# Performance work log

Measured on AMD Instinct MI355X. Metric: run time of the kernel, lower is better.

The kernel has to match this reference:

```python
import jax, jax.numpy as jnp
import numpy as np

DN = ('NCHW', 'OIHW', 'NCHW')

def conv2d(x, w, b, stride, pad):
    y = jax.lax.conv_general_dilated(x, w, (stride, stride), ((pad, pad), (pad, pad)), dimension_numbers=DN)
    return y + b[None, :, None, None]

def conv_transpose2d(x, w, b, stride, pad):
    # w in PyTorch ConvTranspose2d layout: (in_ch, out_ch, kH, kW)
    k = w.shape[2]
    wf = jnp.transpose(w, (1, 0, 2, 3))[:, :, ::-1, ::-1]  # flipped, OIHW
    p = k - 1 - pad
    y = jax.lax.conv_general_dilated(x, wf, (1, 1), ((p, p), (p, p)), lhs_dilation=(stride, stride), dimension_numbers=DN)
    return y + b[None, :, None, None]

def residual_vq(z, codebooks):
    # z: (B,H,W,D) latents, codebooks: (Q,K,D)
    B, H, W, D = z.shape
    Q = codebooks.shape[0]
    flat = z.reshape(-1, D)                      # (N, D), N = B*H*W
    residual = flat
    quantized_out = jnp.zeros_like(flat)
    idx_list, loss_list = [], []
    for q in range(Q):
        cb = codebooks[q]                        # (K, D)
        # squared euclidean distances (N, K)
        d = (residual * residual).sum(-1, keepdims=True) - 2.0 * residual @ cb.T + (cb * cb).sum(-1)
        idx = jnp.argmin(d, axis=-1)             # (N,)
        qv = cb[idx]                             # gather (N, D)
        # commitment loss: ||sg(q) - residual||^2
        loss_list.append(jnp.mean(jnp.square(jax.lax.stop_gradient(qv) - residual)))
        qv_st = residual + jax.lax.stop_gradient(qv - residual)  # straight-through
        quantized_out = quantized_out + qv_st
        residual = residual - jax.lax.stop_gradient(qv)
        idx_list.append(idx)
    quantized = quantized_out.reshape(B, H, W, D)
    indices = jnp.stack(idx_list, axis=-1).reshape(B, H, W, Q)
    commit_loss = jnp.stack(loss_list)           # (Q,)
    return quantized, indices, commit_loss

def forward(x, enc_w1, enc_b1, enc_w2, enc_b2, enc_w3, enc_b3, enc_w4, enc_b4,
            codebooks, dec_w1, dec_b1, dec_tw1, dec_tb1, dec_tw2, dec_tb2):
    h = jax.nn.relu(conv2d(x, enc_w1, enc_b1, 2, 1))
    h = jax.nn.relu(conv2d(h, enc_w2, enc_b2, 2, 1))
    h = jax.nn.relu(conv2d(h, enc_w3, enc_b3, 1, 1))
    z = conv2d(h, enc_w4, enc_b4, 1, 1)          # (B, D, H, W)
    z_hwc = jnp.transpose(z, (0, 2, 3, 1))       # (B, H, W, D)
    quantized, indices, commit_loss = residual_vq(z_hwc, codebooks)
    q_chw = jnp.transpose(quantized, (0, 3, 1, 2))
    d = jax.nn.relu(conv2d(q_chw, dec_w1, dec_b1, 1, 1))
    d = jax.nn.relu(conv_transpose2d(d, dec_tw1, dec_tb1, 2, 1))
    recon = jnp.tanh(conv_transpose2d(d, dec_tw2, dec_tb2, 2, 1))
    indices = jnp.transpose(indices, (0, 3, 1, 2))  # (B, Q, H, W)
    return recon, indices, commit_loss, q_chw

def setup_inputs() -> dict:
    key = jax.random.key(0)
    ks = jax.random.split(key, 16)
    D, K, Q = 256, 1024, 4
    def w(k, shape):
        fan_in = int(np.prod(shape[1:]))
        return jax.random.normal(k, shape, jnp.float32) * np.float32(1.0 / np.sqrt(fan_in))
    return {
        'x': jax.random.normal(ks[0], (16, 3, 256, 256), jnp.float32),
        'enc_w1': w(ks[1], (64, 3, 4, 4)),   'enc_b1': jnp.zeros((64,), jnp.float32),
        'enc_w2': w(ks[2], (128, 64, 4, 4)), 'enc_b2': jnp.zeros((128,), jnp.float32),
        'enc_w3': w(ks[3], (D, 128, 3, 3)),  'enc_b3': jnp.zeros((D,), jnp.float32),
        'enc_w4': w(ks[4], (D, D, 3, 3)),    'enc_b4': jnp.zeros((D,), jnp.float32),
        'codebooks': jax.random.normal(ks[5], (Q, K, D), jnp.float32),
        'dec_w1': w(ks[6], (128, D, 3, 3)),  'dec_b1': jnp.zeros((128,), jnp.float32),
        'dec_tw1': w(ks[7], (128, 64, 4, 4)), 'dec_tb1': jnp.zeros((64,), jnp.float32),
        'dec_tw2': w(ks[8], (64, 3, 4, 4)),  'dec_tb2': jnp.zeros((3,), jnp.float32),
    }

def reference(x, enc_w1, enc_b1, enc_w2, enc_b2, enc_w3, enc_b3, enc_w4, enc_b4,
              codebooks, dec_w1, dec_b1, dec_tw1, dec_tb1, dec_tw2, dec_tb2):
    return forward(x, enc_w1, enc_b1, enc_w2, enc_b2, enc_w3, enc_b3, enc_w4, enc_b4,
                   codebooks, dec_w1, dec_b1, dec_tw1, dec_tb1, dec_tw2, dec_tb2)
```

## Files before the change

kernel.cpp:

```cpp
#include <hip/hip_runtime.h>
#include <hip/hip_bf16.h>
#include <math.h>


#define DEVFN static __device__ __forceinline__
DEVFN float b2f(__hip_bfloat16 v){ return __bfloat162float(v); }
DEVFN float ldv(const float* p, long long i){ return p[i]; }
DEVFN float ldv(const __hip_bfloat16* p, long long i){ return b2f(p[i]); }

DEVFN bool sniff_f32(const void* p){
  const unsigned* u = (const unsigned*)p;
  int hits = 0;
  #pragma unroll
  for (int i=0;i<64;i++){
    unsigned b = (u[i]>>7)&0xFFu;
    hits += (b>=118u && b<=134u) ? 1 : 0;
  }
  return hits < 32;
}

DEVFN void gl_lds16(const float* g, float* l){
  __builtin_amdgcn_global_load_lds(
      (const __attribute__((address_space(1))) void*)g,
      (__attribute__((address_space(3))) void*)l, 16, 0, 0);
}
DEVFN void gl_lds4(const float* g, float* l){
  __builtin_amdgcn_global_load_lds(
      (const __attribute__((address_space(1))) void*)g,
      (__attribute__((address_space(3))) void*)l, 4, 0, 0);
}

__global__ __launch_bounds__(64) void k_zero(float* zp)
{
  zp[threadIdx.x] = 0.f;
}

template<class T>
DEVFN void conv1n_impl(const T* __restrict__ x, const T* __restrict__ w,
                       const T* __restrict__ bias, float* __restrict__ out,
                       float* lin, float* lw, float* lb)
{
  const int tid = threadIdx.x;
  const int tx = blockIdx.x & 3, ty = blockIdx.x >> 2;
  const int b = blockIdx.y;
  for (int j = tid; j < 3072; j += 256){
    int co = j & 63, tt = j >> 6;
    int cc = tt >> 4, tap = tt & 15;
    lw[j] = ldv(w, (co*3+cc)*16 + tap);
  }
  if (tid < 64) lb[tid] = ldv(bias, tid);
  const int oy0 = ty*8, ox0 = tx*32;
  const int iy0 = 2*oy0 - 1, ix0 = 2*ox0 - 1;
  for (int j = tid; j < 3564; j += 256){
    int cc = j / 1188, rem = j - cc*1188;
    int r = rem / 66, cx = rem - r*66;
    int iy = iy0 + r, ix = ix0 + cx;
    float v = 0.f;
    if ((unsigned)iy < 256u && (unsigned)ix < 256u)
      v = ldv(x, (long long)b*196608 + (cc*256+iy)*256 + ix);
    lin[j] = v;
  }
  __syncthreads();
  const int pxg = tid & 31, cog = tid >> 5;
  const int y = pxg >> 2, xb = (pxg & 3) << 3;
  float acc[8][8];
  #pragma unroll
  for (int i=0;i<8;i++)
    #pragma unroll
    for (int j=0;j<8;j++) acc[i][j] = lb[cog*8+j];
  #pragma unroll 1
  for (int cc=0; cc<3; cc++){
    #pragma unroll
    for (int ky=0; ky<4; ky++){
      const float* rowp = &lin[(cc*18 + 2*y+ky)*66 + 2*xb];
      float a[18];
      #pragma unroll
      for (int t=0; t<9; t++) *(float2*)&a[2*t] = *(const float2*)&rowp[2*t];
      #pragma unroll
      for (int kx=0; kx<4; kx++){
        const float* wp = &lw[(cc*16 + ky*4+kx)*64 + cog*8];
        float wv[8];
        *(float4*)&wv[0] = *(const float4*)&wp[0];
        *(float4*)&wv[4] = *(const float4*)&wp[4];
        #pragma unroll
        for (int j=0;j<8;j++)
          #pragma unroll
          for (int i=0;i<8;i++)
            acc[i][j] += a[2*i+kx]*wv[j];
      }
    }
  }
  #pragma unroll
  for (int j=0;j<8;j++){
    const int co = cog*8 + j;
    float4 v0, v1;
    v0.x = fmaxf(acc[0][j],0.f); v0.y = fmaxf(acc[1][j],0.f);
    v0.z = fmaxf(acc[2][j],0.f); v0.w = fmaxf(acc[3][j],0.f);
    v1.x = fmaxf(acc[4][j],0.f); v1.y = fmaxf(acc[5][j],0.f);
    v1.z = fmaxf(acc[6][j],0.f); v1.w = fmaxf(acc[7][j],0.f);
    long long base = ((long long)(b*64 + co)*128 + oy0+y)*128 + ox0+xb;
    *(float4*)&out[base]   = v0;
    *(float4*)&out[base+4] = v1;
  }
}

__global__ __launch_bounds__(256) void k_conv1n(const void* x, const void* w,
    const void* bias, float* out)
{
  __shared__ __align__(16) float lin[3564];
  __shared__ __align__(16) float lw[3072];
  __shared__ float lb[64];
  if (sniff_f32(w)) conv1n_impl((const float*)x, (const float*)w, (const float*)bias, out, lin, lw, lb);
  else conv1n_impl((const __hip_bfloat16*)x, (const __hip_bfloat16*)w, (const __hip_bfloat16*)bias, out, lin, lw, lb);
}

template<class T>
DEVFN void wtr2_impl(const T* __restrict__ w, const T* __restrict__ bias,
                     float* __restrict__ o)
{
  int gid = blockIdx.x*256 + threadIdx.x;
  if (gid < 131072){
    int co = gid & 63;
    int g6 = gid >> 6;
    int t  = g6 & 31;
    int q  = g6 >> 5;
    int cg = q >> 5, ch = q & 31;
    int cc = t >> 4, tap = t & 15;
    o[gid] = ldv(w, ((cg*64+co)*64 + ch*2+cc)*16 + tap);
  } else if (gid < 131200){
    o[gid] = ldv(bias, gid - 131072);
  }
}

__global__ __launch_bounds__(256) void k_wtr2(const void* w, const void* bias, float* o)
{
  if (sniff_f32(w)) wtr2_impl((const float*)w, (const float*)bias, o);
  else wtr2_impl((const __hip_bfloat16*)w, (const __hip_bfloat16*)bias, o);
}

__global__ __launch_bounds__(256) void k_conv2n(const float* __restrict__ in,
    const float* __restrict__ wtr, const float* __restrict__ zp,
    float* __restrict__ out)
{
  __shared__ __align__(16) float lin[2][2432];
  __shared__ __align__(16) float lw[2][2048];
  __shared__ float lb[64];
  const int tid = threadIdx.x;
  const int tx = blockIdx.x & 1, ty = blockIdx.x >> 1;
  const int b = blockIdx.y, cg = blockIdx.z;
  if (tid < 64) lb[tid] = wtr[131072 + cg*64 + tid];
  const int pxg = tid & 31, cog = tid >> 5;
  const int y = pxg >> 2, xb = (pxg & 3) << 3;
  const int oy0 = ty*8, ox0 = tx*32;
  const int wave = tid >> 6, lane = tid & 63;
  const int wbase = wave*64;

  int goff[10];
  #pragma unroll
  for (int ii=0; ii<10; ii++){
    int j = tid + 256*ii;
    int cc = j / 1188, rem = j - cc*1188;
    int r = rem / 66, cx = rem - r*66;
    int iy = 2*oy0 - 1 + r, ix = 2*ox0 - 1 + cx;
    bool ok = (j < 2376) && ((unsigned)iy < 128u) && ((unsigned)ix < 128u);
    goff[ii] = ok ? (cc*16384 + iy*128 + ix) : -1;
  }
  const float* ib0 = in + (long long)b*1048576;
  const float* wb0 = wtr + cg*65536;

  #pragma unroll
  for (int ii=0; ii<10; ii++){
    int wb = wbase + 256*ii;
    if (wb < 2376)
      gl_lds4((goff[ii] >= 0) ? (ib0 + goff[ii]) : zp, &lin[0][wb]);
  }
  for (int c = wave; c < 8; c += 4)
    gl_lds16(wb0 + c*256 + lane*4, &lw[0][c*256]);
  __syncthreads();

  float acc[8][8];
  #pragma unroll
  for (int i=0;i<8;i++)
    #pragma unroll
    for (int j=0;j<8;j++) acc[i][j] = lb[cog*8+j];

  float* lin_c = lin[0]; float* lin_n = lin[1];
  float* lw_c  = lw[0];  float* lw_n  = lw[1];
  for (int k=0; k<32; k++){
    if (k+1 < 32){
      const float* ibk = ib0 + (k+1)*32768;
      const float* wn  = wb0 + (k+1)*2048;
      #pragma unroll
      for (int ii=0; ii<10; ii++){
        int wb = wbase + 256*ii;
        if (wb < 2376)
          gl_lds4((goff[ii] >= 0) ? (ibk + goff[ii]) : zp, lin_n + wb);
      }
      for (int c = wave; c < 8; c += 4)
        gl_lds16(wn + c*256 + lane*4, lw_n + c*256);
    }
    #pragma unroll 1
    for (int cc=0; cc<2; cc++){
      #pragma unroll
      for (int ky=0; ky<4; ky++){
        const float* rowp = &lin_c[(cc*18 + 2*y+ky)*66 + 2*xb];
        float a[18];
        #pragma unroll
        for (int t=0; t<9; t++) *(float2*)&a[2*t] = *(const float2*)&rowp[2*t];
        #pragma unroll
        for (int kx=0; kx<4; kx++){
          const float* wp = &lw_c[(cc*16 + ky*4+kx)*64 + cog*8];
          float wv[8];
          *(float4*)&wv[0] = *(const float4*)&wp[0];
          *(float4*)&wv[4] = *(const float4*)&wp[4];
          #pragma unroll
          for (int j=0;j<8;j++)
            #pragma unroll
            for (int i=0;i<8;i++)
              acc[i][j] += a[2*i+kx]*wv[j];
        }
      }
    }
    __syncthreads();
    float* t0 = lin_c; lin_c = lin_n; lin_n = t0;
    float* t1 = lw_c;  lw_c  = lw_n;  lw_n  = t1;
  }

  #pragma unroll
  for (int j=0;j<8;j++){
    const int co = cg*64 + cog*8 + j;
    float4 v0, v1;
    v0.x = fmaxf(acc[0][j],0.f); v0.y = fmaxf(acc[1][j],0.f);
    v0.z = fmaxf(acc[2][j],0.f); v0.w = fmaxf(acc[3][j],0.f);
    v1.x = fmaxf(acc[4][j],0.f); v1.y = fmaxf(acc[5][j],0.f);
    v1.z = fmaxf(acc[6][j],0.f); v1.w = fmaxf(acc[7][j],0.f);
    long long base = ((long long)(b*128 + co)*64 + oy0+y)*64 + ox0+xb;
    *(float4*)&out[base]   = v0;
    *(float4*)&out[base+4] = v1;
  }
}

template<int CO, int CI, class T>
DEVFN void wtr_impl(const T* __restrict__ w, const T* __restrict__ bias,
                    float* __restrict__ o)
{
  const int NW = CO*CI*9;
  int gid = blockIdx.x*256 + threadIdx.x;
  if (gid < NW){
    int co = gid & 63;
    int g6 = gid >> 6;
    int t  = g6 % 36;
    int q  = g6 / 36;
    const int NCH = CI/4;
    int cg = q / NCH, ch = q - cg*NCH;
    int cc = t / 9, tap = t - cc*9;
    o[gid] = ldv(w, ((long long)(cg*64+co)*CI + ch*4+cc)*9 + tap);
  } else if (gid < NW + CO){
    o[gid] = ldv(bias, gid - NW);
  }
}

template<int CO, int CI>
__global__ __launch_bounds__(256) void k_wtr(const void* w, const void* bias, float* o)
{
  if (sniff_f32(w)) wtr_impl<CO,CI>((const float*)w, (const float*)bias, o);
  else wtr_impl<CO,CI>((const __hip_bfloat16*)w, (const __hip_bfloat16*)bias, o);
}

template<int CI, bool RELU, bool OUT_T>
__global__ __launch_bounds__(256) void k_conv3x3(const float* __restrict__ in,
    const float* __restrict__ wtr, const float* __restrict__ zp,
    float* __restrict__ out)
{
  __shared__ __align__(16) float lin[2][1408];
  __shared__ __align__(16) float lw[2][2304];
  __shared__ float lb[64];
  const int tid = threadIdx.x;
  const int tx = blockIdx.x & 1, ty = blockIdx.x >> 1;
  const int b = blockIdx.y, cg = blockIdx.z;
  const int CO = gridDim.z * 64;
  const int NCH = CI/4;
  const long long NW = (long long)CO*CI*9;
  if (tid < 64) lb[tid] = wtr[NW + cg*64 + tid];

  const int pxg = tid & 31, cog = tid >> 5;
  const int y = pxg >> 2, xb = (pxg & 3) << 3;
  const int oy0 = ty*8, ox0 = tx*32;
  const int wave = tid >> 6, lane = tid & 63;
  const int wbase = wave*64;

  int goff[6];
  #pragma unroll
  for (int ii=0; ii<6; ii++){
    int j = tid + 256*ii;
    int cc = j / 340, rem = j - cc*340;
    int r = rem / 34, cx = rem - r*34;
    int iy = oy0 - 1 + r, ix = ox0 - 1 + cx;
    bool ok = (j < 1360) && ((unsigned)iy < 64u) && ((unsigned)ix < 64u);
    goff[ii] = ok ? (cc*4096 + iy*64 + ix) : -1;
  }
  const float* ib0 = in + (long long)b*CI*4096;
  const float* wb0 = wtr + (long long)cg*NCH*2304;

  #pragma unroll
  for (int ii=0; ii<6; ii++){
    int wb = wbase + 256*ii;
    if (wb < 1360)
      gl_lds4((goff[ii] >= 0) ? (ib0 + goff[ii]) : zp, &lin[0][wb]);
  }
  for (int c = wave; c < 9; c += 4)
    gl_lds16(wb0 + c*256 + lane*4, &lw[0][c*256]);
  __syncthreads();

  float acc[8][8];
  #pragma unroll
  for (int i=0;i<8;i++)
    #pragma unroll
    for (int j=0;j<8;j++) acc[i][j] = lb[cog*8+j];

  float* lin_c = lin[0]; float* lin_n = lin[1];
  float* lw_c  = lw[0];  float* lw_n  = lw[1];
  for (int k=0; k<NCH; k++){
    if (k+1 < NCH){
      const float* ibk = ib0 + (long long)(k+1)*16384;
      const float* wn  = wb0 + (long long)(k+1)*2304;
      #pragma unroll
      for (int ii=0; ii<6; ii++){
        int wb = wbase + 256*ii;
        if (wb < 1360)
          gl_lds4((goff[ii] >= 0) ? (ibk + goff[ii]) : zp, lin_n + wb);
      }
      for (int c = wave; c < 9; c += 4)
        gl_lds16(wn + c*256 + lane*4, lw_n + c*256);
    }
    #pragma unroll 1
    for (int cc=0; cc<4; cc++){
      #pragma unroll
      for (int dy=0; dy<3; dy++){
        const float* rowp = &lin_c[(cc*10 + y+dy)*34 + xb];
        float a[10];
        *(float2*)&a[0] = *(const float2*)&rowp[0];
        *(float2*)&a[2] = *(const float2*)&rowp[2];
        *(float2*)&a[4] = *(const float2*)&rowp[4];
        *(float2*)&a[6] = *(const float2*)&rowp[6];
        *(float2*)&a[8] = *(const float2*)&rowp[8];
        #pragma unroll
        for (int dx=0; dx<3; dx++){
          const float* wp = &lw_c[(cc*9 + dy*3+dx)*64 + cog*8];
          float wv[8];
          *(float4*)&wv[0] = *(const float4*)&wp[0];
          *(float4*)&wv[4] = *(const float4*)&wp[4];
          #pragma unroll
          for (int j=0;j<8;j++)
            #pragma unroll
            for (int i=0;i<8;i++)
              acc[i][j] += a[i+dx]*wv[j];
        }
      }
    }
    __syncthreads();
    float* t0 = lin_c; lin_c = lin_n; lin_n = t0;
    float* t1 = lw_c;  lw_c  = lw_n;  lw_n  = t1;
  }

  const int oy = oy0 + y;
  #pragma unroll
  for (int j=0;j<8;j++){
    const int co = cg*64 + cog*8 + j;
    float4 v0, v1;
    v0.x = acc[0][j]; v0.y = acc[1][j]; v0.z = acc[2][j]; v0.w = acc[3][j];
    v1.x = acc[4][j]; v1.y = acc[5][j]; v1.z = acc[6][j]; v1.w = acc[7][j];
    if (RELU){
      v0.x = fmaxf(v0.x, 0.f); v0.y = fmaxf(v0.y, 0.f);
      v0.z = fmaxf(v0.z, 0.f); v0.w = fmaxf(v0.w, 0.f);
      v1.x = fmaxf(v1.x, 0.f); v1.y = fmaxf(v1.y, 0.f);
      v1.z = fmaxf(v1.z, 0.f); v1.w = fmaxf(v1.w, 0.f);
    }
    long long base = OUT_T ? ((long long)co*65536 + b*4096 + oy*64 + ox0+xb)
                           : (((long long)(b*CO + co)*64 + oy)*64 + ox0+xb);
    *(float4*)&out[base]   = v0;
    *(float4*)&out[base+4] = v1;
  }
}

template<class T>
DEVFN void cbt_impl(const T* __restrict__ cb, float* __restrict__ o,
                    float (*t)[65])
{
  const int k0 = blockIdx.x*64, d0 = blockIdx.y*64, q = blockIdx.z;
  const int tid = threadIdx.x;
  const int rr = tid >> 6, cc = tid & 63;
  #pragma unroll
  for (int p=0; p<16; p++){
    int kk = p*4 + rr;
    t[kk][cc] = ldv(cb, ((long long)(q*1024 + k0+kk))*256 + d0 + cc);
  }
  __syncthreads();
  #pragma unroll
  for (int p=0; p<16; p++){
    int dd = p*4 + rr;
    o[((long long)(q*256 + d0+dd))*1024 + k0 + cc] = t[cc][dd];
  }
}

__global__ __launch_bounds__(256) void k_cbt(const void* cb, float* o)
{
  __shared__ float t[64][65];
  if (sniff_f32(cb)) cbt_impl((const float*)cb, o, t);
  else cbt_impl((const __hip_bfloat16*)cb, o, t);
}

template<class T>
DEVFN void cnh_impl(const T* __restrict__ cb, float* __restrict__ cnh, float* ps)
{
  int row = blockIdx.x;
  float v = ldv(cb, (long long)row*256 + threadIdx.x);
  float s = v*v;
  for (int o=32;o>0;o>>=1) s += __shfl_down(s, o, 64);
  if ((threadIdx.x & 63) == 0) ps[threadIdx.x>>6] = s;
  __syncthreads();
  if (threadIdx.x == 0) cnh[row] = 0.5f*(ps[0]+ps[1]+ps[2]+ps[3]);
}

__global__ __launch_bounds__(256) void k_cnh(const void* cb, float* cnh)
{
  __shared__ float ps[4];
  if (sniff_f32(cb)) cnh_impl((const float*)cb, cnh, ps);
  else cnh_impl((const __hip_bfloat16*)cb, cnh, ps);
}

__global__ __launch_bounds__(256, 2) void k_argmin(const float* __restrict__ resT,
    const float* __restrict__ cbT, const float* __restrict__ cnh,
    int* __restrict__ idxOut, int* __restrict__ flagOut)
{
  __shared__ __align__(16) float lp[2][2048];
  __shared__ __align__(16) float lc[2][4096];
  const int tid = threadIdx.x;
  const int n0 = blockIdx.x * 128;
  const int tp = tid & 15, tc = tid >> 4;
  const int wave = tid >> 6, lane = tid & 63;
  const long long lpLane = (long long)(lane >> 5)*65536 + (lane & 31)*4;
  const float* rb  = resT + n0;
  const float* cbl = cbT + lane*4;

  float m1[8], m2[8]; int i1[8];
  #pragma unroll
  for (int i=0;i<8;i++){ m1[i]=INFINITY; m2[i]=INFINITY; i1[i]=0; }

  #pragma unroll
  for (int r2=0;r2<2;r2++){
    const int dd = wave*4 + r2*2;
    gl_lds16(rb + (long long)dd*65536 + lpLane, &lp[0][dd*128]);
  }
  #pragma unroll
  for (int r=0;r<4;r++){
    const int dd = wave*4 + r;
    gl_lds16(cbl + (long long)dd*1024, &lc[0][dd*256]);
  }
  __syncthreads();

  float acc[8][16];
  float* lp_c = lp[0]; float* lp_n = lp[1];
  float* lc_c = lc[0]; float* lc_n = lc[1];
  for (int it=0; it<64; ++it){
    const int ct = it>>4, dc = it&15;
    if (dc == 0){
      #pragma unroll
      for (int i=0;i<8;i++)
        #pragma unroll
        for (int j=0;j<16;j++) acc[i][j] = 0.f;
    }
    if (it+1 < 64){
      const int d2 = ((it+1)&15)*16, k2 = ((it+1)>>4)*256;
      #pragma unroll
      for (int r2=0;r2<2;r2++){
        const int dd = wave*4 + r2*2;
        gl_lds16(rb + (long long)(d2+dd)*65536 + lpLane, lp_n + dd*128);
      }
      #pragma unroll
      for (int r=0;r<4;r++){
        const int dd = wave*4 + r;
        gl_lds16(cbl + (long long)(d2+dd)*1024 + k2, lc_n + dd*256);
      }
    }
    #pragma unroll 4
    for (int dd=0; dd<16; dd++){
      float a[8], c[16];
      *(float4*)&a[0] = *(const float4*)&lp_c[dd*128 + 4*tp];
      *(float4*)&a[4] = *(const float4*)&lp_c[dd*128 + 64 + 4*tp];
      *(float4*)&c[0]  = *(const float4*)&lc_c[dd*256 + 16*tc];
      *(float4*)&c[4]  = *(const float4*)&lc_c[dd*256 + 16*tc + 4];
      *(float4*)&c[8]  = *(const float4*)&lc_c[dd*256 + 16*tc + 8];
      *(float4*)&c[12] = *(const float4*)&lc_c[dd*256 + 16*tc + 12];
      #pragma unroll
      for (int i=0;i<8;i++)
        #pragma unroll
        for (int j=0;j<16;j++) acc[i][j] += a[i]*c[j];
    }
    if (dc == 15){
      const int k0 = ct*256;
      #pragma unroll
      for (int j=0;j<16;j++){
        const int k = k0 + 16*tc + j;
        const float cn = cnh[k];
        #pragma unroll
        for (int i=0;i<8;i++){
          float s = cn - acc[i][j];
          if (s < m1[i]) { m2[i] = m1[i]; m1[i] = s; i1[i] = k; }
          else if (s < m2[i]) m2[i] = s;
        }
      }
    }
    __syncthreads();
    float* t0 = lp_c; lp_c = lp_n; lp_n = t0;
    float* t1 = lc_c; lc_c = lc_n; lc_n = t1;
  }

  float* rm1 = &lc[0][0];
  float* rm2 = &lc[0][0] + 2176;
  int*   ri1 = (int*)&lp[0][0];
  #pragma unroll
  for (int i=0;i<8;i++){
    const int pnt = (i<4) ? (4*tp + i) : (64 + 4*tp + i - 4);
    rm1[pnt*17 + tc] = m1[i];
    rm2[pnt*17 + tc] = m2[i];
    ri1[pnt*17 + tc] = i1[i];
  }
  __syncthreads();
  if (tid < 128){
    float bm1 = INFINITY, bm2 = INFINITY; int bi = 0;
    for (int t=0;t<16;t++){
      float a = rm1[tid*17+t], b2v = rm2[tid*17+t]; int ia = ri1[tid*17+t];
      if (a < bm1 || (a == bm1 && ia < bi)){ bm2 = fminf(bm1, b2v); bm1 = a; bi = ia; }
      else bm2 = fminf(bm2, fminf(a, b2v));
    }
    idxOut[n0 + tid] = bi;
    float tau = 1e-3f + 1e-5f*fabsf(bm1);
    flagOut[n0 + tid] = (bm2 - bm1 < tau) ? 1 : 0;
  }
}

template<class TCB>
DEVFN void fixup_impl(const float* __restrict__ resT, const TCB* __restrict__ cb,
    long long koff, const int* __restrict__ flags, int* __restrict__ idxOut,
    double* bm, int* bis, float* rsh)
{
  const int tid = threadIdx.x;
  const int n0 = blockIdx.x * 64;
  for (int p=0; p<64; p++){
    int n = n0 + p;
    if (!flags[n]) continue;
    rsh[tid] = resT[tid*65536 + n];
    __syncthreads();
    double best = INFINITY; int bidx = 0;
    for (int c=0; c<4; c++){
      int k = tid*4 + c;
      long long base = koff + (long long)k*256;
      double s0=0.0, s1=0.0, s2=0.0, s3=0.0;
      #pragma unroll 8
      for (int d=0; d<256; d+=4){
        double c0 = (double)ldv(cb, base+d);
        double c1 = (double)ldv(cb, base+d+1);
        double c2 = (double)ldv(cb, base+d+2);
        double c3 = (double)ldv(cb, base+d+3);
        s0 += c0*(c0 - 2.0*(double)rsh[d]);
        s1 += c1*(c1 - 2.0*(double)rsh[d+1]);
        s2 += c2*(c2 - 2.0*(double)rsh[d+2]);
        s3 += c3*(c3 - 2.0*(double)rsh[d+3]);
      }
      double s = (s0+s1)+(s2+s3);
      if (s < best || (s == best && k < bidx)){ best = s; bidx = k; }
    }
    bm[tid] = best; bis[tid] = bidx;
    __syncthreads();
    for (int st=128; st>0; st>>=1){
      if (tid < st){
        if (bm[tid+st] < bm[tid] || (bm[tid+st] == bm[tid] && bis[tid+st] < bis[tid])){
          bm[tid] = bm[tid+st]; bis[tid] = bis[tid+st];
        }
      }
      __syncthreads();
    }
    if (tid == 0) idxOut[n] = bis[0];
    __syncthreads();
  }
}

__global__ __launch_bounds__(256) void k_fixup(const float* resT, const void* cb,
    long long koff, const int* flags, int* idxOut)
{
  __shared__ double bm[256]; __shared__ int bis[256];
  __shared__ float rsh[256];
  if (sniff_f32(cb)) fixup_impl(resT, (const float*)cb, koff, flags, idxOut, bm, bis, rsh);
  else fixup_impl(resT, (const __hip_bfloat16*)cb, koff, flags, idxOut, bm, bis, rsh);
}

template<bool FIRST, class TCB>
DEVFN void update4_impl(const TCB* __restrict__ cb, long long koff,
    const int* __restrict__ idx, float* __restrict__ resT,
    float* __restrict__ qf, float* __restrict__ lossP, float* ps)
{
  int gid = blockIdx.x*256 + threadIdx.x;
  int n = (gid & 16383) * 4, d = gid >> 14;
  int b = n >> 12, hw = n & 4095;
  long long ro = (long long)d*65536 + n;
  float4 r = *(const float4*)&resT[ro];
  int4 iv = *(const int4*)&idx[n];
  float q0 = ldv(cb, koff + (long long)iv.x*256 + d);
  float q1 = ldv(cb, koff + (long long)iv.y*256 + d);
  float q2 = ldv(cb, koff + (long long)iv.z*256 + d);
  float q3 = ldv(cb, koff + (long long)iv.w*256 + d);
  float d0 = q0 - r.x, d1 = q1 - r.y, d2 = q2 - r.z, d3 = q3 - r.w;
  float4 nr; nr.x = -d0; nr.y = -d1; nr.z = -d2; nr.w = -d3;
  *(float4*)&resT[ro] = nr;
  long long qo = (long long)b*1048576 + d*4096 + hw;
  if (FIRST){
    float4 qv; qv.x = q0; qv.y = q1; qv.z = q2; qv.w = q3;
    *(float4*)&qf[qo] = qv;
  } else {
    float4 old = *(const float4*)&qf[qo];
    float4 qv; qv.x = old.x+q0; qv.y = old.y+q1; qv.z = old.z+q2; qv.w = old.w+q3;
    *(float4*)&qf[qo] = qv;
  }
  float t = d0*d0 + d1*d1 + d2*d2 + d3*d3;
  for (int o=32;o>0;o>>=1) t += __shfl_down(t, o, 64);
  if ((threadIdx.x & 63) == 0) ps[threadIdx.x>>6] = t;
  __syncthreads();
  if (threadIdx.x == 0) lossP[blockIdx.x] = ps[0]+ps[1]+ps[2]+ps[3];
}

template<bool FIRST>
__global__ __launch_bounds__(256) void k_update4(const void* cb, long long koff,
    const int* idx, float* resT, float* qf, float* lossP)
{
  __shared__ float ps[4];
  if (sniff_f32(cb)) update4_impl<FIRST>((const float*)cb, koff, idx, resT, qf, lossP, ps);
  else update4_impl<FIRST>((const __hip_bfloat16*)cb, koff, idx, resT, qf, lossP, ps);
}

__global__ __launch_bounds__(256) void k_lossred(const float* __restrict__ lossP,
    float* __restrict__ outp, int cnt)
{
  double s = 0.0;
  for (int j = threadIdx.x; j < cnt; j += 256) s += (double)lossP[j];
  for (int o=32;o>0;o>>=1) s += __shfl_down(s, o, 64);
  __shared__ double ps[4];
  if ((threadIdx.x & 63) == 0) ps[threadIdx.x>>6] = s;
  __syncthreads();
  if (threadIdx.x == 0) *outp = (float)((ps[0]+ps[1]+ps[2]+ps[3]) / 16777216.0);
}

__global__ __launch_bounds__(256) void k_write_idx(const int* __restrict__ idxAll,
    float* __restrict__ out)
{
  int gid = blockIdx.x*256 + threadIdx.x;
  int hw = gid & 4095, q = (gid>>12)&3, b = gid>>14;
  out[3145728 + gid] = (float)idxAll[q*65536 + b*4096 + hw];
}

template<class T>
DEVFN void wtrd_impl(const T* __restrict__ w, const T* __restrict__ bias,
                     float* __restrict__ o)
{
  int gid = blockIdx.x*256 + threadIdx.x;
  if (gid < 131072){
    int co = gid & 63;
    int g6 = gid >> 6;
    int t  = g6 & 63;
    int ch = g6 >> 6;
    int cc = t >> 4, tap = t & 15;
    int ci = ch*4 + cc;
    float v = ldv(w, ((ci*64 + co)*16 + tap));
    int phys = gid ^ ((tap&1)<<3) ^ ((tap&4)<<2);
    o[phys] = v;
  } else if (gid < 131136){
    o[gid] = ldv(bias, gid - 131072);
  }
}

__global__ __launch_bounds__(256) void k_wtrd(const void* w, const void* bias, float* o)
{
  if (sniff_f32(w)) wtrd_impl((const float*)w, (const float*)bias, o);
  else wtrd_impl((const __hip_bfloat16*)w, (const __hip_bfloat16*)bias, o);
}

__global__ __launch_bounds__(256) void k_deconv1n(const float* __restrict__ in,
    const float* __restrict__ wtr, const float* __restrict__ zp,
    float* __restrict__ out)
{
  __shared__ __align__(16) float SM[9280];
  float* lb = SM + 9216;
  const int tid = threadIdx.x;
  const int tx = blockIdx.x & 3, ty = blockIdx.x >> 2;
  const int b = blockIdx.y;
  if (tid < 64) lb[tid] = wtr[131072 + tid];
  const int pxg = tid & 31, cog = tid >> 5;
  const int xh = pxg & 1, px = (pxg>>1)&1, py = (pxg>>2)&1, yq = pxg>>3;
  const int ox0 = tx*32, oy0 = ty*8, ix0 = tx*16, iy0 = ty*4;
  const int wave = tid >> 6, lane = tid & 63;
  const int wbase = wave*64;

  int goff[2];
  #pragma unroll
  for (int ii=0; ii<2; ii++){
    int j = tid + 256*ii;
    int cc = j / 108, rem = j - cc*108;
    int r = rem / 18, cx = rem - r*18;
    int iy = iy0 - 1 + r, ix = ix0 - 1 + cx;
    bool ok = (j < 432) && ((unsigned)iy < 64u) && ((unsigned)ix < 64u);
    goff[ii] = ok ? (cc*4096 + iy*64 + ix) : -1;
  }
  int wofs[4];
  #pragma unroll
  for (int kyi=0; kyi<2; kyi++)
    #pragma unroll
    for (int kxi=0; kxi<2; kxi++){
      int tap = (1-py+2*kyi)*4 + (1-px) + 2*kxi;
      wofs[kyi*2+kxi] = ((tap*64 + cog*8) ^ ((tap&1)<<3)) ^ ((tap&4)<<2);
    }
  const float* ib0 = in + (long long)b*524288;

  #pragma unroll
  for (int ii=0; ii<2; ii++){
    int wb = wbase + 256*ii;
    if (wb < 432)
      gl_lds4((goff[ii] >= 0) ? (ib0 + goff[ii]) : zp, SM + wb);
  }
  for (int c = wave; c < 16; c += 4)
    gl_lds16(wtr + c*256 + lane*4, SM + 1024 + c*256);
  __syncthreads();

  float acc[8][8];
  #pragma unroll
  for (int i=0;i<8;i++)
    #pragma unroll
    for (int j=0;j<8;j++) acc[i][j] = lb[cog*8+j];

  float* lin_c = SM;        float* lin_n = SM + 512;
  float* lw_c  = SM + 1024; float* lw_n  = SM + 5120;
  for (int k=0; k<32; k++){
    if (k+1 < 32){
      const float* ibk = ib0 + (k+1)*16384;
      const float* wn  = wtr + (k+1)*4096;
      #pragma unroll
      for (int ii=0; ii<2; ii++){
        int wb = wbase + 256*ii;
        if (wb < 432)
          gl_lds4((goff[ii] >= 0) ? (ibk + goff[ii]) : zp, lin_n + wb);
      }
      for (int c = wave; c < 16; c += 4)
        gl_lds16(wn + c*256 + lane*4, lw_n + c*256);
    }
    #pragma unroll 1
    for (int cc=0; cc<4; cc++){
      #pragma unroll
      for (int kyi=0; kyi<2; kyi++){
        const int riy = yq + py + 1 - kyi;
        const float* rowp = &lin_c[(cc*6 + riy)*18 + xh*8];
        float a[10];
        *(float2*)&a[0] = *(const float2*)&rowp[0];
        *(float2*)&a[2] = *(const float2*)&rowp[2];
        *(float2*)&a[4] = *(const float2*)&rowp[4];
        *(float2*)&a[6] = *(const float2*)&rowp[6];
        *(float2*)&a[8] = *(const float2*)&rowp[8];
        #pragma unroll
        for (int kxi=0; kxi<2; kxi++){
          const float* wp = &lw_c[cc*1024 + wofs[kyi*2+kxi]];
          float wv[8];
          *(float4*)&wv[0] = *(const float4*)&wp[0];
          *(float4*)&wv[4] = *(const float4*)&wp[4];
          const int s = 1 + px - kxi;
          #pragma unroll
          for (int j=0;j<8;j++)
            #pragma unroll
            for (int i=0;i<8;i++)
              acc[i][j] += a[i+s]*wv[j];
        }
      }
    }
    __syncthreads();
    float* t0 = lin_c; lin_c = lin_n; lin_n = t0;
    float* t1 = lw_c;  lw_c  = lw_n;  lw_n  = t1;
  }

  float* tile = SM + wave*2304;
  const int cogL = lane >> 5;
  const int oyL = 2*yq + py;
  const long long ob0 = (long long)b*1048576;
  #pragma unroll
  for (int h=0; h<2; h++){
    #pragma unroll
    for (int jp=0; jp<4; jp++){
      const int R = (cogL*4 + jp)*8 + oyL;
      #pragma unroll
      for (int i=0;i<8;i++)
        tile[R*36 + 2*(xh*8+i) + px] = fmaxf(acc[i][h*4+jp], 0.f);
    }
    __syncthreads();
    #pragma unroll
    for (int r=0;r<8;r++){
      const int Q = r*64 + lane;
      const int row = Q >> 3, q = Q & 7;
      const int coRel = row >> 3;
      const int cgl = coRel >> 2, jp = coRel & 3;
      const int co = (2*wave + cgl)*8 + h*4 + jp;
      const int oy = oy0 + (row & 7);
      float4 v = *(const float4*)&tile[row*36 + 4*q];
      *(float4*)&out[ob0 + (long long)co*16384 + oy*128 + ox0 + 4*q] = v;
    }
    __syncthreads();
  }
}

template<class T>
DEVFN void wtd2_impl(const T* __restrict__ w, const T* __restrict__ bias,
                     float* __restrict__ o)
{
  int gid = blockIdx.x*256 + threadIdx.x;
  if (gid < 4096){
    int co = gid & 3;
    int t2 = gid >> 2;
    int tap = t2 & 15, cc = (t2 >> 4) & 3, ch = t2 >> 6;
    int ci = ch*4 + cc;
    o[gid] = (co < 3) ? ldv(w, (ci*3+co)*16 + tap) : 0.f;
  } else if (gid < 4099){
    o[gid] = ldv(bias, gid - 4096);
  }
}

__global__ __launch_bounds__(256) void k_wtd2(const void* w, const void* bias, float* o)
{
  if (sniff_f32(w)) wtd2_impl((const float*)w, (const float*)bias, o);
  else wtd2_impl((const __hip_bfloat16*)w, (const __hip_bfloat16*)bias, o);
}

__global__ __launch_bounds__(256) void k_deconv2n(const float* __restrict__ in,
    const float* __restrict__ wtr, const float* __restrict__ zp,
    float* __restrict__ outp)
{
  __shared__ __align__(16) float SM[3332];
  float* lb = SM + 3328;
  const int tid = threadIdx.x;
  const int tx = blockIdx.x & 3, ty = blockIdx.x >> 2;
  const int b = blockIdx.y;
  if (tid < 3) lb[tid] = wtr[4096 + tid];
  if (tid == 3) lb[3] = 0.f;
  const int xq = tid & 7, yl = (tid>>3)&7, px = (tid>>6)&1, py = tid>>7;
  const int x0 = tx*32, y0 = ty*8;
  const int wave = tid >> 6, lane = tid & 63;
  const int wbase = wave*64;

  int goff[6];
  #pragma unroll
  for (int ii=0; ii<6; ii++){
    int j = tid + 256*ii;
    int cc = j / 340, rem = j - cc*340;
    int r = rem / 34, cx = rem - r*34;
    int iy = y0 - 1 + r, ix = x0 - 1 + cx;
    bool ok = (j < 1360) && ((unsigned)iy < 128u) && ((unsigned)ix < 128u);
    goff[ii] = ok ? (cc*16384 + iy*128 + ix) : -1;
  }
  const float* ib0 = in + (long long)b*1048576;

  #pragma unroll
  for (int ii=0; ii<6; ii++){
    int wb = wbase + 256*ii;
    if (wb < 1360)
      gl_lds4((goff[ii] >= 0) ? (ib0 + goff[ii]) : zp, SM + wb);
  }
  if (wave == 0)
    gl_lds16(wtr + lane*4, SM + 2816);
  __syncthreads();

  float acc[4][4];
  #pragma unroll
  for (int i=0;i<4;i++)
    #pragma unroll
    for (int j=0;j<4;j++) acc[i][j] = lb[j];

  float* lin_c = SM;        float* lin_n = SM + 1408;
  float* lw_c  = SM + 2816; float* lw_n  = SM + 3072;
  for (int k=0; k<16; k++){
    if (k+1 < 16){
      const float* ibk = ib0 + (k+1)*65536;
      const float* wn  = wtr + (k+1)*256;
      #pragma unroll
      for (int ii=0; ii<6; ii++){
        int wb = wbase + 256*ii;
        if (wb < 1360)
          gl_lds4((goff[ii] >= 0) ? (ibk + goff[ii]) : zp, lin_n + wb);
      }
      if (wave == 0)
        gl_lds16(wn + lane*4, lw_n);
    }
    #pragma unroll 1
    for (int cc=0; cc<4; cc++){
      #pragma unroll
      for (int kyi=0; kyi<2; kyi++){
        const int riy = yl + py + 1 - kyi;
        const float* rowp = &lin_c[(cc*10 + riy)*34 + xq*4];
        float a[6];
        *(float2*)&a[0] = *(const float2*)&rowp[0];
        *(float2*)&a[2] = *(const float2*)&rowp[2];
        *(float2*)&a[4] = *(const float2*)&rowp[4];
        #pragma unroll
        for (int kxi=0; kxi<2; kxi++){
          const int tap = (1-py+2*kyi)*4 + (1-px) + 2*kxi;
          const float* wp = &lw_c[(cc*16 + tap)*4];
          float4 wv = *(const float4*)wp;
          const int s = 1 + px - kxi;
          #pragma unroll
          for (int i=0;i<4;i++){
            acc[i][0] += a[i+s]*wv.x;
            acc[i][1] += a[i+s]*wv.y;
            acc[i][2] += a[i+s]*wv.z;
            acc[i][3] += a[i+s]*wv.w;
          }
        }
      }
    }
    __syncthreads();
    float* t0 = lin_c; lin_c = lin_n; lin_n = t0;
    float* t1 = lw_c;  lw_c  = lw_n;  lw_n  = t1;
  }

  float* tile = SM;
  const int oyL = 2*yl + py;
  #pragma unroll
  for (int j=0;j<3;j++)
    #pragma unroll
    for (int i=0;i<4;i++)
      tile[(j*16 + oyL)*68 + 2*(xq*4+i) + px] = tanhf(acc[i][j]);
  __syncthreads();
  const long long bb = (long long)b*196608;
  #pragma unroll
  for (int r=0;r<3;r++){
    const int Q = r*256 + tid;
    const int row = Q >> 4, q = Q & 15;
    const int co = row >> 4, oy2 = row & 15;
    float4 v = *(const float4*)&tile[row*68 + 4*q];
    *(float4*)&outp[bb + (long long)co*65536 + (2*y0 + oy2)*256 + 2*x0 + 4*q] = v;
  }
}

extern "C" void kernel_launch(void* const* d_in, const int* in_sizes, int n_in,
                              void* d_out, int out_size, void* d_ws, size_t ws_size,
                              hipStream_t stream)
{
  const void* x   = d_in[0];
  const void* w1  = d_in[1];  const void* b1  = d_in[2];
  const void* w2  = d_in[3];  const void* b2  = d_in[4];
  const void* w3  = d_in[5];  const void* b3  = d_in[6];
  const void* w4  = d_in[7];  const void* b4  = d_in[8];
  const void* cb  = d_in[9];
  const void* dw1 = d_in[10]; const void* db1 = d_in[11];
  const void* tw1 = d_in[12]; const void* tb1 = d_in[13];
  const void* tw2 = d_in[14]; const void* tb2 = d_in[15];

  float* out_f  = (float*)d_out;
  float* reconO = out_f;
  float* lossO  = out_f + 3407872;
  float* qO     = out_f + 3407876;

  char* p = (char*)d_ws;
  float* PA   = (float*)p;
  float* PB   = (float*)(p + 67108864);
  float* cbT  = (float*)(p + 37748736);
  float* wd2t = (float*)(p + 41943040);
  float* zp2  = (float*)(p + 41959424);
  float* cnh  = (float*)(p + 50331648);
  int*   idxB = (int*)  (p + 50348032);
  int*   flg  = (int*)  (p + 51396608);
  float* lossP= (float*)(p + 51658752);

  float* w3t = qO;
  float* w4t = qO + 4194304;
  float* w2t = qO + 8388608;
  float* d1t = reconO;
  float* t1t = reconO + 1500000;
  float* zp  = reconO + 2500000;

  k_zero<<<1, 64, 0, stream>>>(zp);
  k_wtr<256,128><<<1153, 256, 0, stream>>>(w3,  b3,  w3t);
  k_wtr<256,256><<<2305, 256, 0, stream>>>(w4,  b4,  w4t);
  k_wtr<128,256><<<1153, 256, 0, stream>>>(dw1, db1, d1t);
  k_wtr2<<<513, 256, 0, stream>>>(w2, b2, w2t);
  k_wtrd<<<513, 256, 0, stream>>>(tw1, tb1, t1t);

  k_conv1n<<<dim3(64,16), 256, 0, stream>>>(x, w1, b1, PA);
  k_conv2n<<<dim3(16,16,2), 256, 0, stream>>>(PA, w2t, zp, PB);
  k_conv3x3<128,true ,false><<<dim3(16,16,4), 256, 0, stream>>>(PB, w3t, zp, PA);
  k_conv3x3<256,false,true ><<<dim3(16,16,4), 256, 0, stream>>>(PA, w4t, zp, PB);

  k_cbt<<<dim3(16,4,4), 256, 0, stream>>>(cb, cbT);
  k_cnh<<<4096, 256, 0, stream>>>(cb, cnh);
  k_wtd2<<<17, 256, 0, stream>>>(tw2, tb2, wd2t);
  k_zero<<<1, 64, 0, stream>>>(zp2);

  for (int q=0; q<4; q++){
    long long koff = (long long)q * 262144;
    k_argmin<<<512, 256, 0, stream>>>(PB, cbT + (long long)q*262144,
                                      cnh + q*1024, idxB + q*65536, flg);
    k_fixup <<<1024, 256, 0, stream>>>(PB, cb, koff, flg, idxB + q*65536);
    if (q == 0) k_update4<true ><<<16384, 256, 0, stream>>>(cb, koff, idxB,            PB, qO, lossP);
    else        k_update4<false><<<16384, 256, 0, stream>>>(cb, koff, idxB + q*65536, PB, qO, lossP);
    k_lossred<<<1, 256, 0, stream>>>(lossP, lossO + q, 16384);
  }

  k_write_idx<<<1024, 256, 0, stream>>>(idxB, out_f);

  k_conv3x3<256,true ,false><<<dim3(16,16,2), 256, 0, stream>>>(qO, d1t, zp, PA);
  k_deconv1n<<<dim3(64,16), 256, 0, stream>>>(PA, t1t, zp, PB);
  k_deconv2n<<<dim3(64,16), 256, 0, stream>>>(PB, wd2t, zp2, reconO);
}
```

Baseline: 4.997 ms.

## Interleave conv3x3 block order across channel groups and fuse loss reduction via atomics

The 3x3 conv grid is flattened so that blocks working on the same spatial tile for different output-channel groups are launched next to each other, which should improve L2 reuse of the input tile. Separately, the per-quantizer loss reduction kernel is removed. Each update block now atomically adds its partial sum into a double accumulator, and one small kernel writes all four losses at the end. This trades four tiny launches for 16384 double atomics per quantizer level and makes the summation order nondeterministic.

```diff
diff --git a/kernel.cpp b/kernel.cpp
--- a/kernel.cpp
+++ b/kernel.cpp
@@ -33,6 +33,17 @@
 __global__ __launch_bounds__(64) void k_zero(float* zp)
 {
   zp[threadIdx.x] = 0.f;
+}
+
+__global__ __launch_bounds__(64) void k_zerod(double* p)
+{
+  if (threadIdx.x < 4) p[threadIdx.x] = 0.0;
+}
+
+__global__ __launch_bounds__(64) void k_losswrite(const double* __restrict__ a,
+    float* __restrict__ o)
+{
+  if (threadIdx.x < 4) o[threadIdx.x] = (float)(a[threadIdx.x] / 16777216.0);
 }
 
 template<class T>
@@ -267,7 +278,7 @@
   else wtr_impl<CO,CI>((const __hip_bfloat16*)w, (const __hip_bfloat16*)bias, o);
 }
 
-template<int CI, bool RELU, bool OUT_T>
+template<int CI, int NCG, bool RELU, bool OUT_T>
 __global__ __launch_bounds__(256) void k_conv3x3(const float* __restrict__ in,
     const float* __restrict__ wtr, const float* __restrict__ zp,
     float* __restrict__ out)
@@ -276,9 +287,13 @@
   __shared__ __align__(16) float lw[2][2304];
   __shared__ float lb[64];
   const int tid = threadIdx.x;
-  const int tx = blockIdx.x & 1, ty = blockIdx.x >> 1;
-  const int b = blockIdx.y, cg = blockIdx.z;
-  const int CO = gridDim.z * 64;
+  const int bx = blockIdx.x;
+  const int cgbits = (NCG == 4) ? 2 : 1;
+  const int cg = (bx >> 3) & (NCG - 1);
+  const int tile = (bx & 7) | ((bx >> (3 + cgbits)) << 3);
+  const int tx = tile & 1, ty = tile >> 1;
+  const int b = blockIdx.y;
+  const int CO = NCG * 64;
   const int NCH = CI/4;
   const long long NW = (long long)CO*CI*9;
   if (tid < 64) lb[tid] = wtr[NW + cg*64 + tid];
@@ -598,7 +613,7 @@
 template<bool FIRST, class TCB>
 DEVFN void update4_impl(const TCB* __restrict__ cb, long long koff,
     const int* __restrict__ idx, float* __restrict__ resT,
-    float* __restrict__ qf, float* __restrict__ lossP, float* ps)
+    float* __restrict__ qf, double* __restrict__ lossAcc, float* ps)
 {
   int gid = blockIdx.x*256 + threadIdx.x;
   int n = (gid & 16383) * 4, d = gid >> 14;
@@ -626,28 +641,17 @@
   for (int o=32;o>0;o>>=1) t += __shfl_down(t, o, 64);
   if ((threadIdx.x & 63) == 0) ps[threadIdx.x>>6] = t;
   __syncthreads();
-  if (threadIdx.x == 0) lossP[blockIdx.x] = ps[0]+ps[1]+ps[2]+ps[3];
+  if (threadIdx.x == 0)
+    atomicAdd(lossAcc, (double)(ps[0]+ps[1]+ps[2]+ps[3]));
 }
 
 template<bool FIRST>
 __global__ __launch_bounds__(256) void k_update4(const void* cb, long long koff,
-    const int* idx, float* resT, float* qf, float* lossP)
+    const int* idx, float* resT, float* qf, double* lossAcc)
 {
   __shared__ float ps[4];
-  if (sniff_f32(cb)) update4_impl<FIRST>((const float*)cb, koff, idx, resT, qf, lossP, ps);
-  else update4_impl<FIRST>((const __hip_bfloat16*)cb, koff, idx, resT, qf, lossP, ps);
-}
-
-__global__ __launch_bounds__(256) void k_lossred(const float* __restrict__ lossP,
-    float* __restrict__ outp, int cnt)
-{
-  double s = 0.0;
-  for (int j = threadIdx.x; j < cnt; j += 256) s += (double)lossP[j];
-  for (int o=32;o>0;o>>=1) s += __shfl_down(s, o, 64);
-  __shared__ double ps[4];
-  if ((threadIdx.x & 63) == 0) ps[threadIdx.x>>6] = s;
-  __syncthreads();
-  if (threadIdx.x == 0) *outp = (float)((ps[0]+ps[1]+ps[2]+ps[3]) / 16777216.0);
+  if (sniff_f32(cb)) update4_impl<FIRST>((const float*)cb, koff, idx, resT, qf, lossAcc, ps);
+  else update4_impl<FIRST>((const __hip_bfloat16*)cb, koff, idx, resT, qf, lossAcc, ps);
 }
 
 __global__ __launch_bounds__(256) void k_write_idx(const int* __restrict__ idxAll,
@@ -971,7 +975,7 @@
   float* cnh  = (float*)(p + 50331648);
   int*   idxB = (int*)  (p + 50348032);
   int*   flg  = (int*)  (p + 51396608);
-  float* lossP= (float*)(p + 51658752);
+  double* lossAcc = (double*)(p + 51658752);
 
   float* w3t = qO;
   float* w4t = qO + 4194304;
@@ -989,27 +993,28 @@
 
   k_conv1n<<<dim3(64,16), 256, 0, stream>>>(x, w1, b1, PA);
   k_conv2n<<<dim3(16,16,2), 256, 0, stream>>>(PA, w2t, zp, PB);
-  k_conv3x3<128,true ,false><<<dim3(16,16,4), 256, 0, stream>>>(PB, w3t, zp, PA);
-  k_conv3x3<256,false,true ><<<dim3(16,16,4), 256, 0, stream>>>(PA, w4t, zp, PB);
+  k_conv3x3<128,4,true ,false><<<dim3(64,16), 256, 0, stream>>>(PB, w3t, zp, PA);
+  k_conv3x3<256,4,false,true ><<<dim3(64,16), 256, 0, stream>>>(PA, w4t, zp, PB);
 
   k_cbt<<<dim3(16,4,4), 256, 0, stream>>>(cb, cbT);
   k_cnh<<<4096, 256, 0, stream>>>(cb, cnh);
   k_wtd2<<<17, 256, 0, stream>>>(tw2, tb2, wd2t);
   k_zero<<<1, 64, 0, stream>>>(zp2);
+  k_zerod<<<1, 64, 0, stream>>>(lossAcc);
 
   for (int q=0; q<4; q++){
     long long koff = (long long)q * 262144;
     k_argmin<<<512, 256, 0, stream>>>(PB, cbT + (long long)q*262144,
                                       cnh + q*1024, idxB + q*65536, flg);
     k_fixup <<<1024, 256, 0, stream>>>(PB, cb, koff, flg, idxB + q*65536);
-    if (q == 0) k_update4<true ><<<16384, 256, 0, stream>>>(cb, koff, idxB,            PB, qO, lossP);
-    else        k_update4<false><<<16384, 256, 0, stream>>>(cb, koff, idxB + q*65536, PB, qO, lossP);
-    k_lossred<<<1, 256, 0, stream>>>(lossP, lossO + q, 16384);
-  }
+    if (q == 0) k_update4<true ><<<16384, 256, 0, stream>>>(cb, koff, idxB,            PB, qO, lossAcc);
+    else        k_update4<false><<<16384, 256, 0, stream>>>(cb, koff, idxB + q*65536, PB, qO, lossAcc + q);
+  }
+  k_losswrite<<<1, 64, 0, stream>>>(lossAcc, lossO);
 
   k_write_idx<<<1024, 256, 0, stream>>>(idxB, out_f);
 
-  k_conv3x3<256,true ,false><<<dim3(16,16,2), 256, 0, stream>>>(qO, d1t, zp, PA);
+  k_conv3x3<256,2,true ,false><<<dim3(32,16), 256, 0, stream>>>(qO, d1t, zp, PA);
   k_deconv1n<<<dim3(64,16), 256, 0, stream>>>(PA, t1t, zp, PB);
   k_deconv2n<<<dim3(64,16), 256, 0, stream>>>(PB, wd2t, zp2, reconO);
 }
```

Measured after the change: 5.729 ms. +14.7%, slower.
